# Kernel tuning notes

Hardware: AMD Instinct MI355X
Metric: run time of the kernel (lower is better)

## Reference

```python
import jax, jax.numpy as jnp
import numpy as np

N = 100_000      # nodes
E = 1_600_000    # edges (avg degree 16)
H = 2            # heads
C = 32           # out channels per head
L = 4            # EGAT layers
IN = 4           # input one-hot dim (node labels)
ECLS = 5         # edge classes (ratings)
SCALE = 0.1


def setup_inputs() -> dict:
    key = jax.random.key(0)
    ks = jax.random.split(key, 8)
    # node labels arange%4 -> equal user (0) / item (1) counts; x is one-hot (input_embedding=False)
    labels = jnp.arange(N) % 4
    x = jax.nn.one_hot(labels, IN, dtype=jnp.float32)
    edge_index = jax.random.randint(ks[0], (2, E), 0, N)
    edge_attr = jax.random.randint(ks[1], (E,), 0, ECLS)
    W0 = jax.random.normal(ks[2], (IN, H * C), dtype=jnp.float32) * SCALE
    W13 = jax.random.normal(ks[3], (L - 1, H * C, H * C), dtype=jnp.float32) * SCALE
    eemb = jax.random.normal(ks[4], (L, ECLS, H * C), dtype=jnp.float32) * SCALE
    att_src = jax.random.normal(ks[5], (L, H, C), dtype=jnp.float32) * SCALE
    att_dst = jax.random.normal(ks[6], (L, H, C), dtype=jnp.float32) * SCALE
    bias = jnp.zeros((L, H * C), dtype=jnp.float32)
    return dict(x=x, W0=W0, W13=W13, eemb=eemb, att_src=att_src,
                att_dst=att_dst, bias=bias, edge_index=edge_index, edge_attr=edge_attr)


def _egat_layer(x, W, eemb_l, a_src, a_dst, b, src, dst, edge_attr):
    # x: [N, Fin] -> h: [N, H, C]
    h = (x @ W).reshape(N, H, C)
    e = eemb_l[edge_attr].reshape(E, H, C)            # per-edge type embedding
    m = h[src] + e                                    # [E, H, C] edge-featured message
    logits = jax.nn.leaky_relu(
        jnp.sum(h[dst] * a_dst, axis=-1) + jnp.sum(m * a_src, axis=-1), 0.2)  # [E, H]
    # ragged softmax over incoming edges of each destination node
    amax = jax.ops.segment_max(logits, dst, num_segments=N)
    amax = jnp.where(jnp.isfinite(amax), amax, 0.0)
    ex = jnp.exp(logits - amax[dst])
    denom = jax.ops.segment_sum(ex, dst, num_segments=N)
    alpha = ex / (denom[dst] + 1e-16)                 # [E, H]
    out = jax.ops.segment_sum(alpha[..., None] * m, dst, num_segments=N)  # [N, H, C]
    return jax.nn.elu(out.reshape(N, H * C) + b)      # concat heads + elu activation


def reference(x, W0, W13, eemb, att_src, att_dst, bias, edge_index, edge_attr):
    src, dst = edge_index[0], edge_index[1]
    h = _egat_layer(x, W0, eemb[0], att_src[0], att_dst[0], bias[0], src, dst, edge_attr)
    for l in range(1, L):
        h = _egat_layer(h, W13[l - 1], eemb[l], att_src[l], att_dst[l], bias[l], src, dst, edge_attr)
    # users are nodes with label 0 (x[:,0]==1), items label 1 (x[:,1]==1);
    # labels were built as arange(N)%4, so user/item indices are static strided slices.
    user_idx = jnp.arange(0, N, 4)
    item_idx = jnp.arange(1, N, 4)
    u = h[user_idx]
    v = h[item_idx]
    return jnp.sum(u * v, axis=-1)  # MF decoder, multiply_by=1
```

## Files before the change

kernel.cpp:

```cpp
#include <hip/hip_runtime.h>
#include <hip/hip_bf16.h>
#include <math.h>

#define N_NODES 100000
#define N_EDGES 1600000
#define NPAIRS 25000
#define HC 64
#define NHEADS 2
#define NLAYERS 4
#define ECLS 5
#define NBUCK 196
#define NBLK 512
#define EPB (N_EDGES / NBLK)
#define NGRP (N_NODES / 16)
#define LIN0_BLOCKS 1024
#define FCAP 12288

typedef __attribute__((ext_vector_type(8))) short short8;
typedef __attribute__((ext_vector_type(4))) float floatx4;
typedef __attribute__((ext_vector_type(4))) unsigned int uintx4;
union F8 { uint4 u; short8 s; };

__device__ inline float bf_lo(unsigned int u) { return __uint_as_float(u << 16); }
__device__ inline float bf_hi(unsigned int u) { return __uint_as_float(u & 0xffff0000u); }
__device__ inline unsigned short f2bf(float f) {
    unsigned int u = __float_as_uint(f);
    u += 0x7FFFu + ((u >> 16) & 1u);
    return (unsigned short)(u >> 16);
}

__global__ void k_chist_lin0(const int* __restrict__ dst, int* __restrict__ bh,
                             const float* __restrict__ in,
                             const float* __restrict__ W,
                             const float* __restrict__ asrc, const float* __restrict__ adst,
                             unsigned short* __restrict__ hcurb,
                             float* __restrict__ ssrc, float* __restrict__ sdst,
                             const float* __restrict__ eemb, float* __restrict__ escore) {
    int tid = threadIdx.x;
    if (blockIdx.x < NBLK) {
        __shared__ int lh[NBUCK];
        int blk = blockIdx.x;
        for (int i = tid; i < NBUCK; i += 256) lh[i] = 0;
        __syncthreads();
        int s = blk * EPB;
        for (int i = tid; i < EPB; i += 256) atomicAdd(&lh[dst[s + i] >> 9], 1);
        __syncthreads();
        for (int i = tid; i < NBUCK; i += 256) bh[i * NBLK + blk] = lh[i];
        return;
    }
    if (blockIdx.x >= NBLK + LIN0_BLOCKS) {
        if (tid < NLAYERS * ECLS * NHEADS) {
            int l = tid / (ECLS * NHEADS);
            int r = tid % (ECLS * NHEADS);
            int c = r >> 1;
            int h = r & 1;
            float s = 0.f;
            const float* ev = eemb + l * ECLS * HC + c * HC + h * 32;
            const float* av = asrc + l * HC + h * 32;
            for (int k = 0; k < 32; ++k) s += ev[k] * av[k];
            escore[tid] = s;
        }
        return;
    }
    int j = tid & 63;
    int wid = ((blockIdx.x - NBLK) * 256 + tid) >> 6;
    int nwaves = LIN0_BLOCKS * 4;

    float w0 = W[0 * HC + j], w1 = W[1 * HC + j], w2 = W[2 * HC + j], w3 = W[3 * HC + j];
    int head = j >> 5;
    int c = j & 31;
    float as = asrc[head * 32 + c];
    float ad = adst[head * 32 + c];

    for (int n = wid; n < N_NODES; n += nwaves) {
        int nu = __builtin_amdgcn_readfirstlane(n);
        float4 r = *(const float4*)(in + (size_t)nu * 4);
        float acc = r.x * w0 + r.y * w1 + r.z * w2 + r.w * w3;
        hcurb[(size_t)nu * HC + j] = f2bf(acc);
        float ps = acc * as;
        float pd = acc * ad;
        for (int off = 16; off > 0; off >>= 1) {
            ps += __shfl_down(ps, off, 32);
            pd += __shfl_down(pd, off, 32);
        }
        if (c == 0) {
            ssrc[nu * 2 + head] = ps;
            sdst[nu * 2 + head] = pd;
        }
    }
}

__global__ void k_s1(const int* __restrict__ bh, int* __restrict__ bbase,
                     int* __restrict__ part) {
    __shared__ int tmp[NBLK];
    int tid = threadIdx.x;
    int i = blockIdx.x * NBLK + tid;
    int v = bh[i];
    tmp[tid] = v;
    __syncthreads();
    for (int off = 1; off < NBLK; off <<= 1) {
        int t = (tid >= off) ? tmp[tid - off] : 0;
        __syncthreads();
        tmp[tid] += t;
        __syncthreads();
    }
    bbase[i] = tmp[tid] - v;
    if (tid == NBLK - 1) part[blockIdx.x] = tmp[NBLK - 1];
}

__global__ void k_cscatter(const int* __restrict__ src, const int* __restrict__ dst,
                           const int* __restrict__ attr, const int* __restrict__ bbase,
                           const int* __restrict__ part, int* __restrict__ bkt) {
    __shared__ int tmp[256];
    __shared__ int cur[NBUCK];
    __shared__ int gadj[NBUCK];
    __shared__ int stage[EPB];
    __shared__ unsigned char stb[EPB];
    int tid = threadIdx.x, blk = blockIdx.x;
    int pv = (tid < NBUCK) ? part[tid] : 0;
    tmp[tid] = pv;
    __syncthreads();
    for (int off = 1; off < 256; off <<= 1) {
        int t = (tid >= off) ? tmp[tid - off] : 0;
        __syncthreads();
        tmp[tid] += t;
        __syncthreads();
    }
    if (tid < NBUCK) gadj[tid] = tmp[tid] - pv;
    if (tid < NBUCK) cur[tid] = 0;
    for (int i = tid + 256; i < NBUCK; i += 256) cur[i] = 0;
    __syncthreads();
    int s0 = blk * EPB;
    for (int i = tid; i < EPB; i += 256) atomicAdd(&cur[dst[s0 + i] >> 9], 1);
    __syncthreads();
    int v = (tid < NBUCK) ? cur[tid] : 0;
    tmp[tid] = v;
    __syncthreads();
    for (int off = 1; off < 256; off <<= 1) {
        int t = (tid >= off) ? tmp[tid - off] : 0;
        __syncthreads();
        tmp[tid] += t;
        __syncthreads();
    }
    int ex = tmp[tid] - v;
    if (tid < NBUCK) {
        cur[tid] = ex;
        gadj[tid] += bbase[tid * NBLK + blk] - ex;
    }
    __syncthreads();
    for (int i = tid; i < EPB; i += 256) {
        int e = s0 + i;
        int d = dst[e];
        int b = d >> 9;
        int pos = atomicAdd(&cur[b], 1);
        stage[pos] = src[e] | (attr[e] << 17) | ((d & 511) << 20);
        stb[pos] = (unsigned char)b;
    }
    __syncthreads();
    for (int i = tid; i < EPB; i += 256)
        bkt[gadj[stb[i]] + i] = stage[i];
}

__global__ void k_fine(const int* __restrict__ part, const int* __restrict__ bkt,
                       int* __restrict__ packed, int* __restrict__ rowstart) {
    __shared__ int hist[512];
    __shared__ int cur[512];
    __shared__ int pscan[512];
    __shared__ int stage[FCAP];
    int b = blockIdx.x, tid = threadIdx.x;
    int pv = (tid < NBUCK) ? part[tid] : 0;
    pscan[tid] = pv;
    __syncthreads();
    for (int off = 1; off < 512; off <<= 1) {
        int t = (tid >= off) ? pscan[tid - off] : 0;
        __syncthreads();
        pscan[tid] += t;
        __syncthreads();
    }
    int base = (b == 0) ? 0 : pscan[b - 1];
    int bend = pscan[b];
    int nb = bend - base;
    hist[tid] = 0;
    __syncthreads();
    for (int i = tid; i < nb; i += 512)
        atomicAdd(&hist[(bkt[base + i] >> 20) & 0x1FF], 1);
    __syncthreads();
    int v = hist[tid];
    for (int off = 1; off < 512; off <<= 1) {
        int t = (tid >= off) ? hist[tid - off] : 0;
        __syncthreads();
        hist[tid] += t;
        __syncthreads();
    }
    int excl = hist[tid] - v;
    int node = (b << 9) + tid;
    if (node <= N_NODES) rowstart[node] = base + excl;
    cur[tid] = excl;
    __syncthreads();
    if (nb <= FCAP) {
        for (int i = tid; i < nb; i += 512) {
            int p = bkt[base + i];
            int r = atomicAdd(&cur[(p >> 20) & 0x1FF], 1);
            stage[r] = p;
        }
        __syncthreads();
        for (int i = tid; i < nb; i += 512) packed[base + i] = stage[i];
    } else {
        for (int i = tid; i < nb; i += 512) {
            int p = bkt[base + i];
            int r = atomicAdd(&cur[(p >> 20) & 0x1FF], 1);
            packed[base + r] = p;
        }
    }
}

__global__ void k_linmfma(const unsigned short* __restrict__ actB,
                          const float* __restrict__ Wl,
                          const float* __restrict__ asrc,
                          const float* __restrict__ adst,
                          unsigned short* __restrict__ hcurb,
                          float* __restrict__ ssrc, float* __restrict__ sdst) {
    __shared__ uint4 WB[512];
    __shared__ unsigned short Cb[4][1024];
    int tid = threadIdx.x;
    int lane = tid & 63;
    int w = tid >> 6;
    int q = lane >> 4;
    int c = lane & 15;

    for (int rid = tid; rid < 512; rid += 256) {
        int kk = rid >> 8;
        int t  = (rid >> 6) & 3;
        int ln = rid & 63;
        int qq = ln >> 4, cc = ln & 15;
        unsigned int u[4];
        #pragma unroll
        for (int jj = 0; jj < 4; ++jj) {
            float v0 = Wl[(kk * 32 + qq * 8 + jj * 2 + 0) * 64 + 16 * t + cc];
            float v1 = Wl[(kk * 32 + qq * 8 + jj * 2 + 1) * 64 + 16 * t + cc];
            u[jj] = (unsigned int)f2bf(v0) | ((unsigned int)f2bf(v1) << 16);
        }
        WB[rid] = make_uint4(u[0], u[1], u[2], u[3]);
    }
    __syncthreads();

    short8 bfr[2][4];
    #pragma unroll
    for (int kk = 0; kk < 2; ++kk)
        #pragma unroll
        for (int t = 0; t < 4; ++t) {
            F8 tmp; tmp.u = WB[(kk * 4 + t) * 64 + lane];
            bfr[kk][t] = tmp.s;
        }

    float as_[4], ad_[4];
    #pragma unroll
    for (int t = 0; t < 4; ++t) {
        as_[t] = asrc[16 * t + c];
        ad_[t] = adst[16 * t + c];
    }

    int wid = (blockIdx.x * 256 + tid) >> 6;
    int nwaves = gridDim.x * 4;

    for (int g = wid; g < NGRP; g += nwaves) {
        int base = g * 16;
        F8 a0, a1;
        a0.u = *(const uint4*)(actB + (size_t)(base + c) * HC + q * 8);
        a1.u = *(const uint4*)(actB + (size_t)(base + c) * HC + 32 + q * 8);

        floatx4 acc[4];
        #pragma unroll
        for (int t = 0; t < 4; ++t) {
            acc[t] = (floatx4){0.f, 0.f, 0.f, 0.f};
            acc[t] = __builtin_amdgcn_mfma_f32_16x16x32_bf16(a0.s, bfr[0][t], acc[t], 0, 0, 0);
            acc[t] = __builtin_amdgcn_mfma_f32_16x16x32_bf16(a1.s, bfr[1][t], acc[t], 0, 0, 0);
        }

        #pragma unroll
        for (int r = 0; r < 4; ++r) {
            float h0s = acc[0][r] * as_[0] + acc[1][r] * as_[1];
            float h1s = acc[2][r] * as_[2] + acc[3][r] * as_[3];
            float h0d = acc[0][r] * ad_[0] + acc[1][r] * ad_[1];
            float h1d = acc[2][r] * ad_[2] + acc[3][r] * ad_[3];
            #pragma unroll
            for (int off = 1; off < 16; off <<= 1) {
                h0s += __shfl_xor(h0s, off, 64);
                h1s += __shfl_xor(h1s, off, 64);
                h0d += __shfl_xor(h0d, off, 64);
                h1d += __shfl_xor(h1d, off, 64);
            }
            if (c == 0) {
                int node = base + q * 4 + r;
                *(float2*)(ssrc + node * 2) = make_float2(h0s, h1s);
                *(float2*)(sdst + node * 2) = make_float2(h0d, h1d);
            }
        }

        #pragma unroll
        for (int t = 0; t < 4; ++t)
            #pragma unroll
            for (int r = 0; r < 4; ++r)
                Cb[w][(q * 4 + r) * 64 + 16 * t + c] = f2bf(acc[t][r]);
        __builtin_amdgcn_wave_barrier();
        const uint4* cf = (const uint4*)&Cb[w][0];
        uint4* gout = (uint4*)(hcurb + (size_t)base * HC);
        gout[lane] = cf[lane];
        gout[64 + lane] = cf[64 + lane];
        __builtin_amdgcn_wave_barrier();
    }
}

template <bool LAST>
__global__ __launch_bounds__(256)
void k_edge2(const int* __restrict__ rowstart, const int* __restrict__ packed,
             const float* __restrict__ ssrc, const float* __restrict__ sdst,
             const float* __restrict__ escore_l,
             const unsigned short* __restrict__ hcurb,
             const float* __restrict__ eemb_l,
             const float* __restrict__ bias_l,
             unsigned short* __restrict__ actnext, float* __restrict__ out) {
    constexpr int SPAN = LAST ? 64 : 32;
    constexpr int CAP  = LAST ? 1440 : 800;
    __shared__ float4 ebuf[CAP];
    __shared__ float  cls[SPAN * 10];
    __shared__ float2 sdl[SPAN];
    __shared__ float2 esc2[ECLS];

    const int tid = threadIdx.x;
    const int n0 = blockIdx.x * SPAN;

    for (int i = tid; i < SPAN * 10; i += 256) cls[i] = 0.f;
    if (tid < ECLS) esc2[tid] = ((const float2*)escore_l)[tid];
    if (tid < SPAN) {
        int nn = n0 + tid; if (nn > N_NODES - 1) nn = N_NODES - 1;
        sdl[tid] = ((const float2*)sdst)[nn];
    }
    int spanEnd = n0 + SPAN; if (spanEnd > N_NODES) spanEnd = N_NODES;
    const int beg = rowstart[n0];
    const int end = rowstart[spanEnd];
    __syncthreads();

    const int nb = end - beg;
    for (int i = tid; i < nb; i += 256) {
        int p = __builtin_nontemporal_load(&packed[beg + i]);
        int dl = ((p >> 20) & 511) - (n0 & 511);
        if (!LAST || ((dl & 2) == 0)) {
            int s = p & 0x1FFFF;
            int a = (p >> 17) & 7;
            float2 sv = *(const float2*)(ssrc + s * 2);
            float2 dv = sdl[dl];
            float2 ev = esc2[a];
            float l0 = dv.x + sv.x + ev.x; l0 = l0 >= 0.f ? l0 : 0.2f * l0;
            float l1 = dv.y + sv.y + ev.y; l1 = l1 >= 0.f ? l1 : 0.2f * l1;
            float w0 = __expf(l0), w1 = __expf(l1);
            if (i < CAP) ebuf[i] = make_float4(__int_as_float(p), w0, w1, 0.f);
            atomicAdd(&cls[dl * 10 + a * 2 + 0], w0);
            atomicAdd(&cls[dl * 10 + a * 2 + 1], w1);
        }
    }
    __syncthreads();

    const int lane = tid & 63;
    const int q = lane & 7;
    const int hh = q >> 2;
    const int slot = (tid >> 6) * 8 + (lane >> 3);
    int myn, pair = 0;
    bool valid = true;
    if (LAST) {
        pair = blockIdx.x * 16 + (slot >> 1);
        valid = pair < NPAIRS;
        myn = n0 + (slot >> 1) * 4 + (slot & 1);
    } else {
        myn = n0 + slot;
    }
    const int b0 = valid ? rowstart[myn] : 0;
    const int b1 = valid ? rowstart[myn + 1] : 0;
    const unsigned short* hb = hcurb + q * 8;

    float4 a0 = make_float4(0.f, 0.f, 0.f, 0.f);
    float4 a1 = make_float4(0.f, 0.f, 0.f, 0.f);

    struct PE { int p; float wt; };
    auto fetch = [&](int i) -> PE {
        PE r;
        int j = i - beg;
        if (j < CAP) {
            float4 t = ebuf[j];
            r.p = __float_as_int(t.x);
            r.wt = hh ? t.z : t.y;
        } else {
            int p = packed[i];
            int aa = (p >> 17) & 7;
            int ss = p & 0x1FFFF;
            int dll = ((p >> 20) & 511) - (n0 & 511);
            float2 dv2 = sdl[dll];
            float2 ev2 = esc2[aa];
            float lg = (hh ? dv2.y : dv2.x) + ssrc[ss * 2 + hh] + (hh ? ev2.y : ev2.x);
            lg = lg >= 0.f ? lg : 0.2f * lg;
            r.p = p;
            r.wt = __expf(lg);
        }
        return r;
    };

#define ACC8(wt, hv) do { \
        a0.x += (wt) * bf_lo((hv).x); a0.y += (wt) * bf_hi((hv).x); \
        a0.z += (wt) * bf_lo((hv).y); a0.w += (wt) * bf_hi((hv).y); \
        a1.x += (wt) * bf_lo((hv).z); a1.y += (wt) * bf_hi((hv).z); \
        a1.z += (wt) * bf_lo((hv).w); a1.w += (wt) * bf_hi((hv).w); \
    } while (0)

    int i = b0;
    for (; i + 4 <= b1; i += 4) {
        PE e0 = fetch(i);
        PE e1 = fetch(i + 1);
        PE e2 = fetch(i + 2);
        PE e3 = fetch(i + 3);
        uint4 h0 = *(const uint4*)(hb + ((e0.p & 0x1FFFF) << 6));
        uint4 h1 = *(const uint4*)(hb + ((e1.p & 0x1FFFF) << 6));
        uint4 h2 = *(const uint4*)(hb + ((e2.p & 0x1FFFF) << 6));
        uint4 h3 = *(const uint4*)(hb + ((e3.p & 0x1FFFF) << 6));
        ACC8(e0.wt, h0);
        ACC8(e1.wt, h1);
        ACC8(e2.wt, h2);
        ACC8(e3.wt, h3);
    }
    for (; i < b1; ++i) {
        PE e0 = fetch(i);
        uint4 h0 = *(const uint4*)(hb + ((e0.p & 0x1FFFF) << 6));
        ACC8(e0.wt, h0);
    }
#undef ACC8

    const int dl = myn - n0;
    float ssum = 0.f;
    const float* ef = eemb_l + q * 8;
    #pragma unroll
    for (int a = 0; a < ECLS; ++a) {
        float c = cls[dl * 10 + a * 2 + hh];
        ssum += c;
        float4 e0 = *(const float4*)(ef + a * HC);
        float4 e1 = *(const float4*)(ef + a * HC + 4);
        a0.x += c * e0.x; a0.y += c * e0.y; a0.z += c * e0.z; a0.w += c * e0.w;
        a1.x += c * e1.x; a1.y += c * e1.y; a1.z += c * e1.z; a1.w += c * e1.w;
    }
    float inv = 1.f / (ssum + 1e-16f);
    float4 bv0 = *(const float4*)(bias_l + q * 8);
    float4 bv1 = *(const float4*)(bias_l + q * 8 + 4);
    float o0 = a0.x * inv + bv0.x; o0 = o0 > 0.f ? o0 : (__expf(o0) - 1.f);
    float o1 = a0.y * inv + bv0.y; o1 = o1 > 0.f ? o1 : (__expf(o1) - 1.f);
    float o2 = a0.z * inv + bv0.z; o2 = o2 > 0.f ? o2 : (__expf(o2) - 1.f);
    float o3 = a0.w * inv + bv0.w; o3 = o3 > 0.f ? o3 : (__expf(o3) - 1.f);
    float o4 = a1.x * inv + bv1.x; o4 = o4 > 0.f ? o4 : (__expf(o4) - 1.f);
    float o5 = a1.y * inv + bv1.y; o5 = o5 > 0.f ? o5 : (__expf(o5) - 1.f);
    float o6 = a1.z * inv + bv1.z; o6 = o6 > 0.f ? o6 : (__expf(o6) - 1.f);
    float o7 = a1.w * inv + bv1.w; o7 = o7 > 0.f ? o7 : (__expf(o7) - 1.f);

    if (!LAST) {
        unsigned int u0 = (unsigned int)f2bf(o0) | ((unsigned int)f2bf(o1) << 16);
        unsigned int u1 = (unsigned int)f2bf(o2) | ((unsigned int)f2bf(o3) << 16);
        unsigned int u2 = (unsigned int)f2bf(o4) | ((unsigned int)f2bf(o5) << 16);
        unsigned int u3 = (unsigned int)f2bf(o6) | ((unsigned int)f2bf(o7) << 16);
        uintx4 uv = (uintx4){u0, u1, u2, u3};
        __builtin_nontemporal_store(uv, (uintx4*)(actnext + (size_t)myn * HC + q * 8));
    } else {
        float pdot = o0 * __shfl_xor(o0, 8, 64)
                   + o1 * __shfl_xor(o1, 8, 64)
                   + o2 * __shfl_xor(o2, 8, 64)
                   + o3 * __shfl_xor(o3, 8, 64)
                   + o4 * __shfl_xor(o4, 8, 64)
                   + o5 * __shfl_xor(o5, 8, 64)
                   + o6 * __shfl_xor(o6, 8, 64)
                   + o7 * __shfl_xor(o7, 8, 64);
        pdot += __shfl_xor(pdot, 1, 64);
        pdot += __shfl_xor(pdot, 2, 64);
        pdot += __shfl_xor(pdot, 4, 64);
        if (valid && ((slot & 1) == 0) && (q == 0)) out[pair] = pdot;
    }
}

extern "C" void kernel_launch(void* const* d_in, const int* in_sizes, int n_in,
                              void* d_out, int out_size, void* d_ws, size_t ws_size,
                              hipStream_t stream) {
    const float* x       = (const float*)d_in[0];
    const float* W0      = (const float*)d_in[1];
    const float* W13     = (const float*)d_in[2];
    const float* eemb    = (const float*)d_in[3];
    const float* att_src = (const float*)d_in[4];
    const float* att_dst = (const float*)d_in[5];
    const float* bias    = (const float*)d_in[6];
    const int*   eidx    = (const int*)d_in[7];
    const int*   eattr   = (const int*)d_in[8];
    float* out = (float*)d_out;

    const int* src = eidx;
    const int* dst = eidx + N_EDGES;

    char* wsb = (char*)d_ws;
    size_t off = 0;
    auto alloc = [&](size_t bytes) { char* p = wsb + off; off += (bytes + 255) & ~(size_t)255; return p; };
    unsigned short* hcurb  = (unsigned short*)alloc((size_t)N_NODES * HC * 2);
    unsigned short* actB   = (unsigned short*)alloc((size_t)N_NODES * HC * 2);
    float*          ssrc   = (float*)alloc((size_t)N_NODES * 2 * 4);
    float*          sdst   = (float*)alloc((size_t)N_NODES * 2 * 4);
    float*          escore = (float*)alloc(NLAYERS * ECLS * NHEADS * 4);
    int*            bh     = (int*)alloc((size_t)NBUCK * NBLK * 4);
    int*            bbase  = (int*)alloc((size_t)NBUCK * NBLK * 4);
    int*            part   = (int*)alloc(256 * 4);
    int*            rowstart = (int*)alloc(((size_t)N_NODES + 1) * 4);
    int*            bkt    = (int*)alloc((size_t)N_EDGES * 4);
    int*            packed = (int*)alloc((size_t)N_EDGES * 4);

    k_chist_lin0<<<NBLK + LIN0_BLOCKS + 1, 256, 0, stream>>>(
        dst, bh, x, W0, att_src, att_dst, hcurb, ssrc, sdst, eemb, escore);
    k_s1<<<NBUCK, NBLK, 0, stream>>>(bh, bbase, part);
    k_cscatter<<<NBLK, 256, 0, stream>>>(src, dst, eattr, bbase, part, bkt);
    k_fine<<<NBUCK, 512, 0, stream>>>(part, bkt, packed, rowstart);

    for (int l = 0; l < NLAYERS; ++l) {
        if (l > 0) {
            k_linmfma<<<512, 256, 0, stream>>>(
                actB, W13 + (size_t)(l - 1) * HC * HC,
                att_src + l * HC, att_dst + l * HC, hcurb, ssrc, sdst);
        }
        const float* esl = escore + l * ECLS * NHEADS;
        const float* el  = eemb + (size_t)l * ECLS * HC;
        const float* bl  = bias + l * HC;
        if (l < NLAYERS - 1)
            k_edge2<false><<<N_NODES / 32, 256, 0, stream>>>(
                rowstart, packed, ssrc, sdst, esl, hcurb, el, bl, actB, nullptr);
        else
            k_edge2<true><<<(NPAIRS + 15) / 16, 256, 0, stream>>>(
                rowstart, packed, ssrc, sdst, esl, hcurb, el, bl, nullptr, out);
    }
}
```

Baseline: 329.2 us.

## Shard node features into four channel slices mapped to XCD pairs for L2 locality

Node features are stored as four 16-channel shards, [shard][node][16], instead of row-major 64 channels. Each edge-aggregation block now handles a single shard (one head half) over a larger node span. The block index is decoded so that each shard is served by a fixed pair of XCDs, which keeps each XCD's gathered working set to a quarter of the feature table and improves L2 hit rates. The cost is that edge logits and exponentials are recomputed once per shard, the final dot product is accumulated with atomics (the output is zeroed in k_s1), and the per-block LDS footprint grows.

```diff
diff --git a/kernel.cpp b/kernel.cpp
--- a/kernel.cpp
+++ b/kernel.cpp
@@ -15,11 +15,13 @@
 #define NGRP (N_NODES / 16)
 #define LIN0_BLOCKS 1024
 #define FCAP 12288
+#define NSHARD 4
 
 typedef __attribute__((ext_vector_type(8))) short short8;
 typedef __attribute__((ext_vector_type(4))) float floatx4;
-typedef __attribute__((ext_vector_type(4))) unsigned int uintx4;
 union F8 { uint4 u; short8 s; };
+
+struct PE { int p; float wt; };
 
 __device__ inline float bf_lo(unsigned int u) { return __uint_as_float(u << 16); }
 __device__ inline float bf_hi(unsigned int u) { return __uint_as_float(u & 0xffff0000u); }
@@ -33,7 +35,7 @@
                              const float* __restrict__ in,
                              const float* __restrict__ W,
                              const float* __restrict__ asrc, const float* __restrict__ adst,
-                             unsigned short* __restrict__ hcurb,
+                             unsigned short* __restrict__ hcurbS,
                              float* __restrict__ ssrc, float* __restrict__ sdst,
                              const float* __restrict__ eemb, float* __restrict__ escore) {
     int tid = threadIdx.x;
@@ -76,7 +78,7 @@
         int nu = __builtin_amdgcn_readfirstlane(n);
         float4 r = *(const float4*)(in + (size_t)nu * 4);
         float acc = r.x * w0 + r.y * w1 + r.z * w2 + r.w * w3;
-        hcurb[(size_t)nu * HC + j] = f2bf(acc);
+        hcurbS[((size_t)(j >> 4) * N_NODES + nu) * 16 + (j & 15)] = f2bf(acc);
         float ps = acc * as;
         float pd = acc * ad;
         for (int off = 16; off > 0; off >>= 1) {
@@ -91,9 +93,11 @@
 }
 
 __global__ void k_s1(const int* __restrict__ bh, int* __restrict__ bbase,
-                     int* __restrict__ part) {
+                     int* __restrict__ part, float* __restrict__ out) {
     __shared__ int tmp[NBLK];
     int tid = threadIdx.x;
+    int gtid = blockIdx.x * NBLK + tid;
+    if (gtid < NPAIRS) out[gtid] = 0.f;
     int i = blockIdx.x * NBLK + tid;
     int v = bh[i];
     tmp[tid] = v;
@@ -128,7 +132,6 @@
     }
     if (tid < NBUCK) gadj[tid] = tmp[tid] - pv;
     if (tid < NBUCK) cur[tid] = 0;
-    for (int i = tid + 256; i < NBUCK; i += 256) cur[i] = 0;
     __syncthreads();
     int s0 = blk * EPB;
     for (int i = tid; i < EPB; i += 256) atomicAdd(&cur[dst[s0 + i] >> 9], 1);
@@ -218,7 +221,7 @@
                           const float* __restrict__ Wl,
                           const float* __restrict__ asrc,
                           const float* __restrict__ adst,
-                          unsigned short* __restrict__ hcurb,
+                          unsigned short* __restrict__ hcurbS,
                           float* __restrict__ ssrc, float* __restrict__ sdst) {
     __shared__ uint4 WB[512];
     __shared__ unsigned short Cb[4][1024];
@@ -301,107 +304,106 @@
         for (int t = 0; t < 4; ++t)
             #pragma unroll
             for (int r = 0; r < 4; ++r)
-                Cb[w][(q * 4 + r) * 64 + 16 * t + c] = f2bf(acc[t][r]);
+                Cb[w][t * 256 + (q * 4 + r) * 16 + c] = f2bf(acc[t][r]);
         __builtin_amdgcn_wave_barrier();
         const uint4* cf = (const uint4*)&Cb[w][0];
-        uint4* gout = (uint4*)(hcurb + (size_t)base * HC);
-        gout[lane] = cf[lane];
-        gout[64 + lane] = cf[64 + lane];
+        #pragma unroll
+        for (int pass = 0; pass < 2; ++pass) {
+            int s = pass * 2 + (lane >> 5);
+            int idx = lane & 31;
+            uint4 v = cf[s * 32 + idx];
+            *(uint4*)(hcurbS + ((size_t)s * N_NODES + base) * 16 + idx * 8) = v;
+        }
         __builtin_amdgcn_wave_barrier();
     }
 }
 
 template <bool LAST>
 __global__ __launch_bounds__(256)
-void k_edge2(const int* __restrict__ rowstart, const int* __restrict__ packed,
+void k_edge3(const int* __restrict__ rowstart, const int* __restrict__ packed,
              const float* __restrict__ ssrc, const float* __restrict__ sdst,
              const float* __restrict__ escore_l,
-             const unsigned short* __restrict__ hcurb,
+             const unsigned short* __restrict__ hcurbS,
              const float* __restrict__ eemb_l,
              const float* __restrict__ bias_l,
              unsigned short* __restrict__ actnext, float* __restrict__ out) {
-    constexpr int SPAN = LAST ? 64 : 32;
-    constexpr int CAP  = LAST ? 1440 : 800;
-    __shared__ float4 ebuf[CAP];
-    __shared__ float  cls[SPAN * 10];
-    __shared__ float2 sdl[SPAN];
-    __shared__ float2 esc2[ECLS];
+    constexpr int SPAN  = LAST ? 256 : 128;
+    constexpr int CAP   = LAST ? 4608 : 2560;
+    constexpr int NSPAN = LAST ? 391 : 782;
+    __shared__ float2 ebuf[CAP];
+    __shared__ float  cls[SPAN * ECLS];
+    __shared__ float  sdl[SPAN];
+    __shared__ float  esc[ECLS];
 
     const int tid = threadIdx.x;
-    const int n0 = blockIdx.x * SPAN;
-
-    for (int i = tid; i < SPAN * 10; i += 256) cls[i] = 0.f;
-    if (tid < ECLS) esc2[tid] = ((const float2*)escore_l)[tid];
-    if (tid < SPAN) {
-        int nn = n0 + tid; if (nn > N_NODES - 1) nn = N_NODES - 1;
-        sdl[tid] = ((const float2*)sdst)[nn];
-    }
-    int spanEnd = n0 + SPAN; if (spanEnd > N_NODES) spanEnd = N_NODES;
+    const int bid = blockIdx.x;
+    const int xcd = bid & 7;
+    const int shard = xcd >> 1;
+    const int spanIdx = (bid >> 3) * 2 + (xcd & 1);
+    if (spanIdx >= NSPAN) return;
+    const int hh = shard >> 1;
+    const int n0 = spanIdx * SPAN;
+    const int nEnd = (n0 + SPAN < N_NODES) ? n0 + SPAN : N_NODES;
+
+    for (int i = tid; i < SPAN * ECLS; i += 256) cls[i] = 0.f;
+    if (tid < ECLS) esc[tid] = escore_l[tid * 2 + hh];
+    for (int i = tid; i < SPAN; i += 256) {
+        int nn = n0 + i; if (nn >= N_NODES) nn = N_NODES - 1;
+        sdl[i] = sdst[nn * 2 + hh];
+    }
     const int beg = rowstart[n0];
-    const int end = rowstart[spanEnd];
+    const int end = rowstart[nEnd];
     __syncthreads();
 
     const int nb = end - beg;
     for (int i = tid; i < nb; i += 256) {
-        int p = __builtin_nontemporal_load(&packed[beg + i]);
+        int p = packed[beg + i];
         int dl = ((p >> 20) & 511) - (n0 & 511);
         if (!LAST || ((dl & 2) == 0)) {
             int s = p & 0x1FFFF;
             int a = (p >> 17) & 7;
-            float2 sv = *(const float2*)(ssrc + s * 2);
-            float2 dv = sdl[dl];
-            float2 ev = esc2[a];
-            float l0 = dv.x + sv.x + ev.x; l0 = l0 >= 0.f ? l0 : 0.2f * l0;
-            float l1 = dv.y + sv.y + ev.y; l1 = l1 >= 0.f ? l1 : 0.2f * l1;
-            float w0 = __expf(l0), w1 = __expf(l1);
-            if (i < CAP) ebuf[i] = make_float4(__int_as_float(p), w0, w1, 0.f);
-            atomicAdd(&cls[dl * 10 + a * 2 + 0], w0);
-            atomicAdd(&cls[dl * 10 + a * 2 + 1], w1);
+            float lg = sdl[dl] + ssrc[s * 2 + hh] + esc[a];
+            lg = lg >= 0.f ? lg : 0.2f * lg;
+            float wt = __expf(lg);
+            if (i < CAP) ebuf[i] = make_float2(__int_as_float(p), wt);
+            atomicAdd(&cls[dl * ECLS + a], wt);
         }
     }
     __syncthreads();
 
     const int lane = tid & 63;
-    const int q = lane & 7;
-    const int hh = q >> 2;
-    const int slot = (tid >> 6) * 8 + (lane >> 3);
-    int myn, pair = 0;
-    bool valid = true;
+    const int p2 = lane & 1;
+    const int slot = (tid >> 6) * 32 + (lane >> 1);
+    int myn, gp = 0;
+    bool valid;
     if (LAST) {
-        pair = blockIdx.x * 16 + (slot >> 1);
-        valid = pair < NPAIRS;
+        gp = spanIdx * 64 + (slot >> 1);
+        valid = gp < NPAIRS;
         myn = n0 + (slot >> 1) * 4 + (slot & 1);
     } else {
         myn = n0 + slot;
+        valid = myn < N_NODES;
     }
     const int b0 = valid ? rowstart[myn] : 0;
     const int b1 = valid ? rowstart[myn + 1] : 0;
-    const unsigned short* hb = hcurb + q * 8;
+    const unsigned short* hb = hcurbS + (size_t)shard * N_NODES * 16 + p2 * 8;
+    const int dl = myn - n0;
 
     float4 a0 = make_float4(0.f, 0.f, 0.f, 0.f);
     float4 a1 = make_float4(0.f, 0.f, 0.f, 0.f);
 
-    struct PE { int p; float wt; };
     auto fetch = [&](int i) -> PE {
-        PE r;
         int j = i - beg;
         if (j < CAP) {
-            float4 t = ebuf[j];
-            r.p = __float_as_int(t.x);
-            r.wt = hh ? t.z : t.y;
-        } else {
-            int p = packed[i];
-            int aa = (p >> 17) & 7;
-            int ss = p & 0x1FFFF;
-            int dll = ((p >> 20) & 511) - (n0 & 511);
-            float2 dv2 = sdl[dll];
-            float2 ev2 = esc2[aa];
-            float lg = (hh ? dv2.y : dv2.x) + ssrc[ss * 2 + hh] + (hh ? ev2.y : ev2.x);
-            lg = lg >= 0.f ? lg : 0.2f * lg;
-            r.p = p;
-            r.wt = __expf(lg);
-        }
-        return r;
+            float2 t = ebuf[j];
+            PE r; r.p = __float_as_int(t.x); r.wt = t.y; return r;
+        }
+        int p = packed[i];
+        int a = (p >> 17) & 7;
+        int s = p & 0x1FFFF;
+        float lg = sdl[dl] + ssrc[s * 2 + hh] + esc[a];
+        lg = lg >= 0.f ? lg : 0.2f * lg;
+        PE r; r.p = p; r.wt = __expf(lg); return r;
     };
 
 #define ACC8(wt, hv) do { \
@@ -417,10 +419,10 @@
         PE e1 = fetch(i + 1);
         PE e2 = fetch(i + 2);
         PE e3 = fetch(i + 3);
-        uint4 h0 = *(const uint4*)(hb + ((e0.p & 0x1FFFF) << 6));
-        uint4 h1 = *(const uint4*)(hb + ((e1.p & 0x1FFFF) << 6));
-        uint4 h2 = *(const uint4*)(hb + ((e2.p & 0x1FFFF) << 6));
-        uint4 h3 = *(const uint4*)(hb + ((e3.p & 0x1FFFF) << 6));
+        uint4 h0 = *(const uint4*)(hb + (size_t)(e0.p & 0x1FFFF) * 16);
+        uint4 h1 = *(const uint4*)(hb + (size_t)(e1.p & 0x1FFFF) * 16);
+        uint4 h2 = *(const uint4*)(hb + (size_t)(e2.p & 0x1FFFF) * 16);
+        uint4 h3 = *(const uint4*)(hb + (size_t)(e3.p & 0x1FFFF) * 16);
         ACC8(e0.wt, h0);
         ACC8(e1.wt, h1);
         ACC8(e2.wt, h2);
@@ -428,17 +430,16 @@
     }
     for (; i < b1; ++i) {
         PE e0 = fetch(i);
-        uint4 h0 = *(const uint4*)(hb + ((e0.p & 0x1FFFF) << 6));
+        uint4 h0 = *(const uint4*)(hb + (size_t)(e0.p & 0x1FFFF) * 16);
         ACC8(e0.wt, h0);
     }
 #undef ACC8
 
-    const int dl = myn - n0;
     float ssum = 0.f;
-    const float* ef = eemb_l + q * 8;
+    const float* ef = eemb_l + shard * 16 + p2 * 8;
     #pragma unroll
     for (int a = 0; a < ECLS; ++a) {
-        float c = cls[dl * 10 + a * 2 + hh];
+        float c = cls[dl * ECLS + a];
         ssum += c;
         float4 e0 = *(const float4*)(ef + a * HC);
         float4 e1 = *(const float4*)(ef + a * HC + 4);
@@ -446,8 +447,9 @@
         a1.x += c * e1.x; a1.y += c * e1.y; a1.z += c * e1.z; a1.w += c * e1.w;
     }
     float inv = 1.f / (ssum + 1e-16f);
-    float4 bv0 = *(const float4*)(bias_l + q * 8);
-    float4 bv1 = *(const float4*)(bias_l + q * 8 + 4);
+    const float* bf = bias_l + shard * 16 + p2 * 8;
+    float4 bv0 = *(const float4*)(bf);
+    float4 bv1 = *(const float4*)(bf + 4);
     float o0 = a0.x * inv + bv0.x; o0 = o0 > 0.f ? o0 : (__expf(o0) - 1.f);
     float o1 = a0.y * inv + bv0.y; o1 = o1 > 0.f ? o1 : (__expf(o1) - 1.f);
     float o2 = a0.z * inv + bv0.z; o2 = o2 > 0.f ? o2 : (__expf(o2) - 1.f);
@@ -458,25 +460,25 @@
     float o7 = a1.w * inv + bv1.w; o7 = o7 > 0.f ? o7 : (__expf(o7) - 1.f);
 
     if (!LAST) {
-        unsigned int u0 = (unsigned int)f2bf(o0) | ((unsigned int)f2bf(o1) << 16);
-        unsigned int u1 = (unsigned int)f2bf(o2) | ((unsigned int)f2bf(o3) << 16);
-        unsigned int u2 = (unsigned int)f2bf(o4) | ((unsigned int)f2bf(o5) << 16);
-        unsigned int u3 = (unsigned int)f2bf(o6) | ((unsigned int)f2bf(o7) << 16);
-        uintx4 uv = (uintx4){u0, u1, u2, u3};
-        __builtin_nontemporal_store(uv, (uintx4*)(actnext + (size_t)myn * HC + q * 8));
+        if (valid) {
+            unsigned int u0 = (unsigned int)f2bf(o0) | ((unsigned int)f2bf(o1) << 16);
+            unsigned int u1 = (unsigned int)f2bf(o2) | ((unsigned int)f2bf(o3) << 16);
+            unsigned int u2 = (unsigned int)f2bf(o4) | ((unsigned int)f2bf(o5) << 16);
+            unsigned int u3 = (unsigned int)f2bf(o6) | ((unsigned int)f2bf(o7) << 16);
+            *(uint4*)(actnext + (size_t)myn * HC + shard * 16 + p2 * 8) =
+                make_uint4(u0, u1, u2, u3);
+        }
     } else {
-        float pdot = o0 * __shfl_xor(o0, 8, 64)
-                   + o1 * __shfl_xor(o1, 8, 64)
-                   + o2 * __shfl_xor(o2, 8, 64)
-                   + o3 * __shfl_xor(o3, 8, 64)
-                   + o4 * __shfl_xor(o4, 8, 64)
-                   + o5 * __shfl_xor(o5, 8, 64)
-                   + o6 * __shfl_xor(o6, 8, 64)
-                   + o7 * __shfl_xor(o7, 8, 64);
-        pdot += __shfl_xor(pdot, 1, 64);
-        pdot += __shfl_xor(pdot, 2, 64);
-        pdot += __shfl_xor(pdot, 4, 64);
-        if (valid && ((slot & 1) == 0) && (q == 0)) out[pair] = pdot;
+        float pd = o0 * __shfl_xor(o0, 2, 64)
+                 + o1 * __shfl_xor(o1, 2, 64)
+                 + o2 * __shfl_xor(o2, 2, 64)
+                 + o3 * __shfl_xor(o3, 2, 64)
+                 + o4 * __shfl_xor(o4, 2, 64)
+                 + o5 * __shfl_xor(o5, 2, 64)
+                 + o6 * __shfl_xor(o6, 2, 64)
+                 + o7 * __shfl_xor(o7, 2, 64);
+        pd += __shfl_xor(pd, 1, 64);
+        if (valid && ((lane & 3) == 0)) atomicAdd(out + gp, pd);
     }
 }
 
@@ -500,7 +502,7 @@
     char* wsb = (char*)d_ws;
     size_t off = 0;
     auto alloc = [&](size_t bytes) { char* p = wsb + off; off += (bytes + 255) & ~(size_t)255; return p; };
-    unsigned short* hcurb  = (unsigned short*)alloc((size_t)N_NODES * HC * 2);
+    unsigned short* hcurbS = (unsigned short*)alloc((size_t)NSHARD * N_NODES * 16 * 2);
     unsigned short* actB   = (unsigned short*)alloc((size_t)N_NODES * HC * 2);
     float*          ssrc   = (float*)alloc((size_t)N_NODES * 2 * 4);
     float*          sdst   = (float*)alloc((size_t)N_NODES * 2 * 4);
@@ -513,8 +515,8 @@
     int*            packed = (int*)alloc((size_t)N_EDGES * 4);
 
     k_chist_lin0<<<NBLK + LIN0_BLOCKS + 1, 256, 0, stream>>>(
-        dst, bh, x, W0, att_src, att_dst, hcurb, ssrc, sdst, eemb, escore);
-    k_s1<<<NBUCK, NBLK, 0, stream>>>(bh, bbase, part);
+        dst, bh, x, W0, att_src, att_dst, hcurbS, ssrc, sdst, eemb, escore);
+    k_s1<<<NBUCK, NBLK, 0, stream>>>(bh, bbase, part, out);
     k_cscatter<<<NBLK, 256, 0, stream>>>(src, dst, eattr, bbase, part, bkt);
     k_fine<<<NBUCK, 512, 0, stream>>>(part, bkt, packed, rowstart);
 
@@ -522,16 +524,16 @@
         if (l > 0) {
             k_linmfma<<<512, 256, 0, stream>>>(
                 actB, W13 + (size_t)(l - 1) * HC * HC,
-                att_src + l * HC, att_dst + l * HC, hcurb, ssrc, sdst);
+                att_src + l * HC, att_dst + l * HC, hcurbS, ssrc, sdst);
         }
         const float* esl = escore + l * ECLS * NHEADS;
         const float* el  = eemb + (size_t)l * ECLS * HC;
         const float* bl  = bias + l * HC;
         if (l < NLAYERS - 1)
-            k_edge2<false><<<N_NODES / 32, 256, 0, stream>>>(
-                rowstart, packed, ssrc, sdst, esl, hcurb, el, bl, actB, nullptr);
+            k_edge3<false><<<8 * 391, 256, 0, stream>>>(
+                rowstart, packed, ssrc, sdst, esl, hcurbS, el, bl, actB, nullptr);
         else
-            k_edge2<true><<<(NPAIRS + 15) / 16, 256, 0, stream>>>(
-                rowstart, packed, ssrc, sdst, esl, hcurb, el, bl, nullptr, out);
-    }
-}
+            k_edge3<true><<<8 * 196, 256, 0, stream>>>(
+                rowstart, packed, ssrc, sdst, esl, hcurbS, el, bl, nullptr, out);
+    }
+}
```

Measured after the change: 458.1 us. 1.39x slower.
